# Performance work log

Measured on AMD Instinct MI355X. Metric: run time of the kernel, lower is better.

## Reference

```python
import jax, jax.numpy as jnp
import numpy as np

H, W = 512, 512
# box_info rows: [pad_left, pad_right, pad_top, pad_bottom, box_w, box_h]
BOX_INFO = np.array([
    [0, 256, 0, 256, 256, 256],
    [64, 256, 32, 160, 192, 320],
    [128, 64, 256, 64, 320, 192],
    [300, 84, 300, 84, 128, 128],
    [64, 64, 128, 128, 384, 256],
    [200, 56, 100, 28, 256, 384],
    [32, 320, 256, 32, 160, 224],
    [256, 32, 320, 32, 224, 160]], dtype=np.int64)
BIG = 100000.0


def _conv(x, w, b):
    # 3x3 SAME conv, NCHW / OIHW, followed by ReLU
    y = jax.lax.conv_general_dilated(x, w, window_strides=(1, 1), padding='SAME',
                                     dimension_numbers=('NCHW', 'OIHW', 'NCHW'))
    return jax.nn.relu(y + b[None, :, None, None])


def _block(x, w1, b1, w2, b2, w3, b3):
    return _conv(_conv(_conv(x, w1, b1), w2, b2), w3, b3)


def _resize_and_pad(x, info):
    l, r, t, btm, bw_, bh_ = [int(v) for v in info]
    x = jax.image.resize(x, (x.shape[0], x.shape[1], bh_, bw_), method='bilinear')
    return jnp.pad(x, ((0, 0), (0, 0), (t, btm), (l, r)))


def setup_inputs() -> dict:
    key = jax.random.key(0)
    ks = jax.random.split(key, 8)
    C, U, N = 64, 64, 8
    s = 0.05
    return {
        'instance_feature': jax.random.normal(ks[0], (N, C, 128, 128), jnp.float32),
        'bg_feature': jax.random.normal(ks[1], (1, C, H, W), jnp.float32),
        'iw1': jax.random.normal(ks[2], (U, C, 3, 3), jnp.float32) * s,
        'ib1': jnp.zeros((U,), jnp.float32),
        'iw2': jax.random.normal(ks[3], (U, U, 3, 3), jnp.float32) * s,
        'ib2': jnp.zeros((U,), jnp.float32),
        'iw3': jax.random.normal(ks[4], (1, U, 3, 3), jnp.float32) * s,
        'ib3': jnp.zeros((1,), jnp.float32),
        'bw1': jax.random.normal(ks[5], (U, C, 3, 3), jnp.float32) * s,
        'bb1': jnp.zeros((U,), jnp.float32),
        'bw2': jax.random.normal(ks[6], (U, U, 3, 3), jnp.float32) * s,
        'bb2': jnp.zeros((U,), jnp.float32),
        'bw3': jax.random.normal(ks[7], (1, U, 3, 3), jnp.float32) * s,
        'bb3': jnp.zeros((1,), jnp.float32),
    }


def reference(instance_feature, bg_feature, iw1, ib1, iw2, ib2, iw3, ib3,
              bw1, bb1, bw2, bb2, bw3, bb3):
    n_inst = instance_feature.shape[0]
    masks, fmaps = [], []
    mask_sum = jnp.zeros((1, 1, H, W), bg_feature.dtype)
    for i in range(n_inst):  # static, structurally distinct per-box shapes
        info = BOX_INFO[i]
        l, t, bw_, bh_ = int(info[0]), int(info[2]), int(info[4]), int(info[5])
        crop = instance_feature[i:i + 1]                      # [1,C,h,w]
        pred_mask = _block(crop, iw1, ib1, iw2, ib2, iw3, ib3)  # [1,1,h,w]
        pred_mask = _resize_and_pad(pred_mask, info)           # [1,1,H,W]
        feat = _resize_and_pad(crop, info)                     # [1,C,H,W]
        m = jnp.zeros((1, 1, H, W), bg_feature.dtype).at[:, :, t:t + bh_, l:l + bw_].set(1.0)
        mask_sum = jnp.clip(mask_sum + m, 0.0, 1.0)
        masks.append(pred_mask)
        fmaps.append(feat)
    pred_bg_mask = _block(bg_feature, bw1, bb1, bw2, bb2, bw3, bb3)  # [1,1,H,W]
    masks.append(pred_bg_mask + (1.0 - mask_sum) * BIG)
    mask_cat = jax.nn.softmax(jnp.concatenate(masks, axis=1), axis=1)  # [1,N+1,H,W]
    fm = jnp.concatenate(fmaps + [bg_feature], axis=0)                 # [N+1,C,H,W]
    # weighted blend: sum_n fm[n] * mask[n]
    out = jnp.sum(fm * jnp.transpose(mask_cat, (1, 0, 2, 3)), axis=0, keepdims=True)
    return out
```

## Files before the change

### kernel.cpp

```cpp
#include <hip/hip_runtime.h>
#include <hip/hip_bf16.h>

typedef __hip_bfloat16 bf16;
typedef unsigned short ushort_t;
typedef unsigned int uint32;

typedef short short4_t __attribute__((ext_vector_type(4)));
typedef short short8_t __attribute__((ext_vector_type(8)));
typedef float float4_t __attribute__((ext_vector_type(4)));

union FragU { short4_t h[2]; short8_t v; };
union Frag16 { short8_t v; short s[8]; uint4 u; };

#define BIG 100000.0f

__global__ __launch_bounds__(256) void wtrans(const float* __restrict__ w,
                                              ushort_t* __restrict__ dst)
{
    int idx = blockIdx.x * 256 + threadIdx.x;
    if (idx < 36864) {
        const int i  = idx & 7;
        const int r  = (idx >> 3) & 63;
        const int f  = idx >> 9;
        const int half = f & 1, mb = (f >> 1) & 3, t = f >> 3;
        const int nn = r & 15, qq = r >> 4;
        const int co = mb * 16 + nn;
        const int ci = half * 32 + qq * 8 + i;
        bf16 h = (bf16)w[(co * 64 + ci) * 9 + t];
        dst[idx] = *(ushort_t*)&h;
    }
}

__global__ __launch_bounds__(256) void nchw_to_nhwc(
    const float* __restrict__ in,
    ushort_t* __restrict__ out,
    int H, int W)
{
    __shared__ ushort_t s[64 * 66];
    const int b = blockIdx.z, y = blockIdx.y, x0 = blockIdx.x * 64;
    const int tid = threadIdx.x;
    const long ibase = (long)b * 64 * H * W + (long)y * W + x0;
    {
        const int x = tid & 63, dc = tid >> 6;
        for (int c = dc; c < 64; c += 4) {
            bf16 h = (bf16)in[ibase + (long)c * H * W + x];
            s[c * 66 + x] = *(ushort_t*)&h;
        }
    }
    __syncthreads();
    {
        const int c = tid & 63, dx = tid >> 6;
        const long obase = ((long)b * H * W + (long)y * W + x0) * 64;
        for (int x = dx; x < 64; x += 4)
            out[obase + (long)x * 64 + c] = s[c * 66 + x];
    }
}

__global__ __launch_bounds__(256, 3) void conv3x3_mfma(
    const ushort_t* __restrict__ in,
    ushort_t* __restrict__ out,
    const ushort_t* __restrict__ wt,
    const float* __restrict__ bias,
    int H, int W)
{
    __shared__ ushort_t s_h[2][324 * 36];

    const int b = blockIdx.z;
    const int x0 = blockIdx.x * 16, y0 = blockIdx.y * 16;
    const int tid = threadIdx.x;
    const int lane = tid & 63, wv = tid >> 6;
    const int n = lane & 15, q = lane >> 4;

    const long img = (long)b * H * W;

    for (int idx = tid; idx < 2592; idx += 256) {
        const int p = idx >> 3, c = idx & 7;
        const int py = p / 18, px = p - py * 18;
        const int gy = y0 - 1 + py, gx = x0 - 1 + px;
        uint4 d = {0u, 0u, 0u, 0u};
        if (gy >= 0 && gy < H && gx >= 0 && gx < W)
            d = *(const uint4*)(in + ((img + (long)gy * W + gx) << 6) + c * 8);
        ushort_t* dp = &s_h[c >> 2][p * 36 + (c & 3) * 8];
        *(uint2*)dp       = make_uint2(d.x, d.y);
        *(uint2*)(dp + 4) = make_uint2(d.z, d.w);
    }
    __syncthreads();

    float4_t acc[4][4];
#pragma unroll
    for (int mb = 0; mb < 4; ++mb)
#pragma unroll
        for (int j = 0; j < 4; ++j) acc[mb][j] = (float4_t){0.f, 0.f, 0.f, 0.f};

#pragma unroll
    for (int half = 0; half < 2; ++half) {
        const ushort_t* sh = s_h[half];
#pragma unroll
        for (int t = 0; t < 9; ++t) {
            const int dy = t / 3, dx = t - dy * 3;
            FragU A[4];
#pragma unroll
            for (int mb = 0; mb < 4; ++mb) {
                const ushort_t* ap = wt + (((t * 4 + mb) * 2 + half) << 9) + (lane << 3);
                A[mb].h[0] = *(const short4_t*)ap;
                A[mb].h[1] = *(const short4_t*)(ap + 4);
            }
#pragma unroll
            for (int j = 0; j < 4; ++j) {
                const int row = wv * 4 + j;
                const ushort_t* p = &sh[((row + dy) * 18 + n + dx) * 36 + q * 8];
                FragU B;
                B.h[0] = *(const short4_t*)p;
                B.h[1] = *(const short4_t*)(p + 4);
#pragma unroll
                for (int mb = 0; mb < 4; ++mb)
                    acc[mb][j] = __builtin_amdgcn_mfma_f32_16x16x32_bf16(
                        A[mb].v, B.v, acc[mb][j], 0, 0, 0);
            }
        }
    }

#pragma unroll
    for (int j = 0; j < 4; ++j) {
        const int gy = y0 + wv * 4 + j, gx = x0 + n;
        ushort_t* op0 = out + ((img + (long)gy * W + gx) << 6);
#pragma unroll
        for (int mb = 0; mb < 4; ++mb) {
            const int co = mb * 16 + q * 4;
            const float4 bv = *(const float4*)(bias + co);
            const float bvr[4] = {bv.x, bv.y, bv.z, bv.w};
            bf16 tmp[4];
#pragma unroll
            for (int r = 0; r < 4; ++r) {
                float v = acc[mb][j][r] + bvr[r];
                v = v > 0.f ? v : 0.f;
                tmp[r] = (bf16)v;
            }
            *(uint2*)(op0 + co) = *(uint2*)tmp;
        }
    }
}

__global__ __launch_bounds__(256) void conv3x3_c1(
    const ushort_t* __restrict__ in,
    float* __restrict__ out,
    const float* __restrict__ w,
    const float* __restrict__ bias,
    int H, int W)
{
    __shared__ ushort_t s_in[324 * 72];
    __shared__ float s_w[576];

    const int b = blockIdx.z;
    const int x0 = blockIdx.x * 16, y0 = blockIdx.y * 16;
    const int tid = threadIdx.x;
    for (int k = tid; k < 576; k += 256) s_w[k] = w[k];

    const long img = (long)b * H * W;
    for (int idx = tid; idx < 2592; idx += 256) {
        const int p = idx >> 3, c = idx & 7;
        const int py = p / 18, px = p - py * 18;
        const int gy = y0 - 1 + py, gx = x0 - 1 + px;
        uint4 d = {0u, 0u, 0u, 0u};
        if (gy >= 0 && gy < H && gx >= 0 && gx < W)
            d = *(const uint4*)(in + ((img + (long)gy * W + gx) << 6) + c * 8);
        *(uint4*)&s_in[p * 72 + c * 8] = d;
    }
    __syncthreads();

    const int px = tid & 15, py = tid >> 4;
    float acc = 0.f;
#pragma unroll
    for (int t = 0; t < 9; ++t) {
        const int dy = t / 3, dx = t - dy * 3;
        const ushort_t* p = &s_in[((py + dy) * 18 + px + dx) * 72];
#pragma unroll
        for (int c8 = 0; c8 < 8; ++c8) {
            Frag16 f;
            f.u = *(const uint4*)(p + c8 * 8);
#pragma unroll
            for (int i = 0; i < 8; ++i) {
                float fv = __uint_as_float(((uint32)(ushort_t)f.s[i]) << 16);
                acc += fv * s_w[(c8 * 8 + i) * 9 + t];
            }
        }
    }
    float v = acc + bias[0];
    v = v > 0.f ? v : 0.f;
    out[img + (long)(y0 + py) * W + x0 + px] = v;
}

#define CPB 16

__global__ __launch_bounds__(256) void fuse_out(
    const float* __restrict__ inst,
    const float* __restrict__ bg,
    const float* __restrict__ m,
    const float* __restrict__ bgm,
    float* __restrict__ out)
{
    const int x = blockIdx.x * 256 + threadIdx.x;
    const int y = blockIdx.y;
    const int c0 = blockIdx.z * CPB;

    constexpr int BL[8]  = {0, 64, 128, 300, 64, 200, 32, 256};
    constexpr int BT[8]  = {0, 32, 256, 300, 128, 100, 256, 320};
    constexpr int BBW[8] = {256, 192, 320, 128, 384, 256, 160, 224};
    constexpr int BBH[8] = {256, 320, 192, 128, 256, 384, 224, 160};

    float logits[9];
    int   o00[8], oxs[8], oys[8];
    float wf00[8], wf01[8], wf10[8], wf11[8];
    bool  ins[8];
    bool any = false;

#pragma unroll
    for (int n = 0; n < 8; ++n) {
        const bool inside = (x >= BL[n]) && (x < BL[n] + BBW[n]) &&
                            (y >= BT[n]) && (y < BT[n] + BBH[n]);
        ins[n] = inside;
        float lg = 0.f;
        o00[n] = 0; oxs[n] = 0; oys[n] = 0;
        wf00[n] = wf01[n] = wf10[n] = wf11[n] = 0.f;
        if (inside) {
            any = true;
            float u = ((x - BL[n]) + 0.5f) * (128.0f / BBW[n]) - 0.5f;
            float v = ((y - BT[n]) + 0.5f) * (128.0f / BBH[n]) - 0.5f;
            u = fminf(fmaxf(u, 0.f), 127.f);
            v = fminf(fmaxf(v, 0.f), 127.f);
            int   xx0 = (int)u;  float fx = u - (float)xx0;
            int   yy0 = (int)v;  float fy = v - (float)yy0;
            o00[n] = yy0 * 128 + xx0;
            oxs[n] = (xx0 < 127) ? 1 : 0;
            oys[n] = (yy0 < 127) ? 128 : 0;
            wf00[n] = (1.f - fx) * (1.f - fy);
            wf01[n] = fx * (1.f - fy);
            wf10[n] = (1.f - fx) * fy;
            wf11[n] = fx * fy;
            const float* mp = m + n * 16384;
            lg = wf00[n] * mp[o00[n]] + wf01[n] * mp[o00[n] + oxs[n]] +
                 wf10[n] * mp[o00[n] + oys[n]] +
                 wf11[n] * mp[o00[n] + oxs[n] + oys[n]];
        }
        logits[n] = lg;
    }
    logits[8] = bgm[y * 512 + x] + (any ? 0.f : BIG);

    float mx = logits[0];
#pragma unroll
    for (int i = 1; i < 9; ++i) mx = fmaxf(mx, logits[i]);
    float wgt[9], s = 0.f;
#pragma unroll
    for (int i = 0; i < 9; ++i) { wgt[i] = __expf(logits[i] - mx); s += wgt[i]; }
    const float inv = 1.f / s;
#pragma unroll
    for (int i = 0; i < 9; ++i) wgt[i] *= inv;

#pragma unroll
    for (int n = 0; n < 8; ++n) {
        wf00[n] *= wgt[n]; wf01[n] *= wgt[n];
        wf10[n] *= wgt[n]; wf11[n] *= wgt[n];
    }

    const long pix = (long)y * 512 + x;

    const float* bgp = bg + (long)c0 * 262144 + pix;
    float o[CPB];
#pragma unroll
    for (int cc = 0; cc < CPB; ++cc)
        o[cc] = wgt[8] * bgp[(long)cc * 262144];

#pragma unroll
    for (int n = 0; n < 8; ++n) {
        if (__any((int)ins[n])) {
            const int   ox  = oxs[n], oy = oys[n], oxy = oxs[n] + oys[n];
            const float w00 = wf00[n], w01 = wf01[n];
            const float w10 = wf10[n], w11 = wf11[n];
            const float* p = inst + (long)(n * 64 + c0) * 16384 + o00[n];
#pragma unroll
            for (int cc = 0; cc < CPB; ++cc) {
                o[cc] += w00 * p[0]  + w01 * p[ox] +
                         w10 * p[oy] + w11 * p[oxy];
                p += 16384;
            }
        }
    }

    float* outp = out + (long)c0 * 262144 + pix;
#pragma unroll
    for (int cc = 0; cc < CPB; ++cc)
        __builtin_nontemporal_store(o[cc], outp + (long)cc * 262144);
}

extern "C" void kernel_launch(void* const* d_in, const int* in_sizes, int n_in,
                              void* d_out, int out_size, void* d_ws, size_t ws_size,
                              hipStream_t stream)
{
    (void)in_sizes; (void)n_in; (void)out_size; (void)ws_size;

    const float* instf = (const float*)d_in[0];
    const float* bgf   = (const float*)d_in[1];
    const float* iw1   = (const float*)d_in[2];
    const float* ib1   = (const float*)d_in[3];
    const float* iw2   = (const float*)d_in[4];
    const float* ib2   = (const float*)d_in[5];
    const float* iw3   = (const float*)d_in[6];
    const float* ib3   = (const float*)d_in[7];
    const float* bw1   = (const float*)d_in[8];
    const float* bb1   = (const float*)d_in[9];
    const float* bw2   = (const float*)d_in[10];
    const float* bb2   = (const float*)d_in[11];
    const float* bw3   = (const float*)d_in[12];
    const float* bb3   = (const float*)d_in[13];

    char* ws = (char*)d_ws;
    ushort_t* instN = (ushort_t*)(ws);
    ushort_t* y2    = (ushort_t*)(ws + 16777216);
    ushort_t* y1    = (ushort_t*)(ws + 33554432);
    ushort_t* bgN   = (ushort_t*)(ws);
    ushort_t* bg1   = (ushort_t*)(ws + 33554432);
    ushort_t* bg2   = (ushort_t*)(ws);
    float*    minst  = (float*)(ws + 67108864);
    float*    bgmask = (float*)(ws + 67633152);
    ushort_t* wt0 = (ushort_t*)(ws + 67633152);
    ushort_t* wt1 = wt0 + 36864;
    ushort_t* wt2 = wt0 + 2 * 36864;
    ushort_t* wt3 = wt0 + 3 * 36864;

    wtrans<<<144, 256, 0, stream>>>(iw1, wt0);
    wtrans<<<144, 256, 0, stream>>>(iw2, wt1);
    wtrans<<<144, 256, 0, stream>>>(bw1, wt2);
    wtrans<<<144, 256, 0, stream>>>(bw2, wt3);

    nchw_to_nhwc<<<dim3(2, 128, 8), 256, 0, stream>>>(instf, instN, 128, 128);
    conv3x3_mfma<<<dim3(8, 8, 8), 256, 0, stream>>>(instN, y1, wt0, ib1, 128, 128);
    conv3x3_mfma<<<dim3(8, 8, 8), 256, 0, stream>>>(y1, y2, wt1, ib2, 128, 128);
    conv3x3_c1  <<<dim3(8, 8, 8), 256, 0, stream>>>(y2, minst, iw3, ib3, 128, 128);

    nchw_to_nhwc<<<dim3(8, 512, 1), 256, 0, stream>>>(bgf, bgN, 512, 512);
    conv3x3_mfma<<<dim3(32, 32, 1), 256, 0, stream>>>(bgN, bg1, wt2, bb1, 512, 512);
    conv3x3_mfma<<<dim3(32, 32, 1), 256, 0, stream>>>(bg1, bg2, wt3, bb2, 512, 512);
    conv3x3_c1  <<<dim3(32, 32, 1), 256, 0, stream>>>(bg2, bgmask, bw3, bb3, 512, 512);

    fuse_out<<<dim3(2, 512, 4), 256, 0, stream>>>(instf, bgf, minst, bgmask, (float*)d_out);
}
```

Before: 405.4 us.

## Merge prep kernels and fuse instance final conv with bg layout transform

Folds the four weight-transform launches and the instance NCHW-to-NHWC transpose into one prep kernel. Merges the instance single-output conv with the background NCHW-to-NHWC transpose into one launch that branches on block id, and remaps the workspace buffers so these stages do not overwrite each other. This cuts launch count and lets independent small stages share the GPU instead of running serially. It also lowers the conv launch-bounds occupancy hint from 3 to 2, trading occupancy for more registers per thread.

```diff
diff --git a/kernel.cpp b/kernel.cpp
--- a/kernel.cpp
+++ b/kernel.cpp
@@ -14,11 +14,22 @@
 
 #define BIG 100000.0f
 
-__global__ __launch_bounds__(256) void wtrans(const float* __restrict__ w,
-                                              ushort_t* __restrict__ dst)
-{
-    int idx = blockIdx.x * 256 + threadIdx.x;
-    if (idx < 36864) {
+__global__ __launch_bounds__(256) void prep(
+    const float* __restrict__ instf,
+    ushort_t* __restrict__ instN,
+    const float* __restrict__ w0, const float* __restrict__ w1,
+    const float* __restrict__ w2, const float* __restrict__ w3,
+    ushort_t* __restrict__ wt)
+{
+    __shared__ ushort_t s[64 * 66];
+    const int id = blockIdx.x;
+    const int tid = threadIdx.x;
+
+    if (id >= 2048) {
+        const int gidx = (id - 2048) * 256 + tid;
+        const int set = gidx / 36864;
+        const int idx = gidx - set * 36864;
+        const float* w = (set == 0) ? w0 : (set == 1) ? w1 : (set == 2) ? w2 : w3;
         const int i  = idx & 7;
         const int r  = (idx >> 3) & 63;
         const int f  = idx >> 9;
@@ -27,36 +38,30 @@
         const int co = mb * 16 + nn;
         const int ci = half * 32 + qq * 8 + i;
         bf16 h = (bf16)w[(co * 64 + ci) * 9 + t];
-        dst[idx] = *(ushort_t*)&h;
-    }
-}
-
-__global__ __launch_bounds__(256) void nchw_to_nhwc(
-    const float* __restrict__ in,
-    ushort_t* __restrict__ out,
-    int H, int W)
-{
-    __shared__ ushort_t s[64 * 66];
-    const int b = blockIdx.z, y = blockIdx.y, x0 = blockIdx.x * 64;
-    const int tid = threadIdx.x;
-    const long ibase = (long)b * 64 * H * W + (long)y * W + x0;
+        wt[set * 36864 + idx] = *(ushort_t*)&h;
+        return;
+    }
+
+    const int b = id >> 8, r = id & 255;
+    const int y = r >> 1, x0 = (r & 1) * 64;
+    const long ibase = (long)b * 64 * 16384 + (long)y * 128 + x0;
     {
         const int x = tid & 63, dc = tid >> 6;
         for (int c = dc; c < 64; c += 4) {
-            bf16 h = (bf16)in[ibase + (long)c * H * W + x];
+            bf16 h = (bf16)instf[ibase + (long)c * 16384 + x];
             s[c * 66 + x] = *(ushort_t*)&h;
         }
     }
     __syncthreads();
     {
         const int c = tid & 63, dx = tid >> 6;
-        const long obase = ((long)b * H * W + (long)y * W + x0) * 64;
+        const long obase = ((long)b * 16384 + (long)y * 128 + x0) * 64;
         for (int x = dx; x < 64; x += 4)
-            out[obase + (long)x * 64 + c] = s[c * 66 + x];
-    }
-}
-
-__global__ __launch_bounds__(256, 3) void conv3x3_mfma(
+            instN[obase + (long)x * 64 + c] = s[c * 66 + x];
+    }
+}
+
+__global__ __launch_bounds__(256, 2) void conv3x3_mfma(
     const ushort_t* __restrict__ in,
     ushort_t* __restrict__ out,
     const ushort_t* __restrict__ wt,
@@ -139,6 +144,80 @@
             *(uint2*)(op0 + co) = *(uint2*)tmp;
         }
     }
+}
+
+__global__ __launch_bounds__(256) void c1i_nchwb(
+    const ushort_t* __restrict__ y2in,
+    float* __restrict__ minst,
+    const float* __restrict__ w,
+    const float* __restrict__ bias,
+    const float* __restrict__ bgf,
+    ushort_t* __restrict__ bgN)
+{
+    __shared__ __align__(16) char smem[48960];
+    const int id = blockIdx.x, tid = threadIdx.x;
+
+    if (id >= 512) {
+        ushort_t* s = (ushort_t*)smem;
+        const int r = id - 512;
+        const int y = r >> 3, x0 = (r & 7) * 64;
+        const long ibase = (long)y * 512 + x0;
+        {
+            const int x = tid & 63, dc = tid >> 6;
+            for (int c = dc; c < 64; c += 4) {
+                bf16 h = (bf16)bgf[ibase + (long)c * 262144 + x];
+                s[c * 66 + x] = *(ushort_t*)&h;
+            }
+        }
+        __syncthreads();
+        {
+            const int c = tid & 63, dx = tid >> 6;
+            const long obase = ((long)y * 512 + x0) * 64;
+            for (int x = dx; x < 64; x += 4)
+                bgN[obase + (long)x * 64 + c] = s[c * 66 + x];
+        }
+        return;
+    }
+
+    ushort_t* s_in = (ushort_t*)smem;
+    float*    s_w  = (float*)(smem + 46656);
+
+    const int b = id >> 6, r = id & 63;
+    const int y0 = (r >> 3) * 16, x0 = (r & 7) * 16;
+    for (int k = tid; k < 576; k += 256) s_w[k] = w[k];
+
+    const long img = (long)b * 16384;
+    for (int idx = tid; idx < 2592; idx += 256) {
+        const int p = idx >> 3, c = idx & 7;
+        const int py = p / 18, px = p - py * 18;
+        const int gy = y0 - 1 + py, gx = x0 - 1 + px;
+        uint4 d = {0u, 0u, 0u, 0u};
+        if (gy >= 0 && gy < 128 && gx >= 0 && gx < 128)
+            d = *(const uint4*)(y2in + ((img + (long)gy * 128 + gx) << 6) + c * 8);
+        *(uint4*)&s_in[p * 72 + c * 8] = d;
+    }
+    __syncthreads();
+
+    const int px = tid & 15, py = tid >> 4;
+    float acc = 0.f;
+#pragma unroll
+    for (int t = 0; t < 9; ++t) {
+        const int dy = t / 3, dx = t - dy * 3;
+        const ushort_t* p = &s_in[((py + dy) * 18 + px + dx) * 72];
+#pragma unroll
+        for (int c8 = 0; c8 < 8; ++c8) {
+            Frag16 f;
+            f.u = *(const uint4*)(p + c8 * 8);
+#pragma unroll
+            for (int i = 0; i < 8; ++i) {
+                float fv = __uint_as_float(((uint32)(ushort_t)f.s[i]) << 16);
+                acc += fv * s_w[(c8 * 8 + i) * 9 + t];
+            }
+        }
+    }
+    float v = acc + bias[0];
+    v = v > 0.f ? v : 0.f;
+    minst[img + (long)(y0 + py) * 128 + x0 + px] = v;
 }
 
 __global__ __launch_bounds__(256) void conv3x3_c1(
@@ -315,11 +394,11 @@
 
     char* ws = (char*)d_ws;
     ushort_t* instN = (ushort_t*)(ws);
-    ushort_t* y2    = (ushort_t*)(ws + 16777216);
-    ushort_t* y1    = (ushort_t*)(ws + 33554432);
-    ushort_t* bgN   = (ushort_t*)(ws);
-    ushort_t* bg1   = (ushort_t*)(ws + 33554432);
-    ushort_t* bg2   = (ushort_t*)(ws);
+    ushort_t* y1    = (ushort_t*)(ws + 16777216);
+    ushort_t* y2    = (ushort_t*)(ws);
+    ushort_t* bgN   = (ushort_t*)(ws + 33554432);
+    ushort_t* bg1   = (ushort_t*)(ws);
+    ushort_t* bg2   = (ushort_t*)(ws + 33554432);
     float*    minst  = (float*)(ws + 67108864);
     float*    bgmask = (float*)(ws + 67633152);
     ushort_t* wt0 = (ushort_t*)(ws + 67633152);
@@ -327,20 +406,12 @@
     ushort_t* wt2 = wt0 + 2 * 36864;
     ushort_t* wt3 = wt0 + 3 * 36864;
 
-    wtrans<<<144, 256, 0, stream>>>(iw1, wt0);
-    wtrans<<<144, 256, 0, stream>>>(iw2, wt1);
-    wtrans<<<144, 256, 0, stream>>>(bw1, wt2);
-    wtrans<<<144, 256, 0, stream>>>(bw2, wt3);
-
-    nchw_to_nhwc<<<dim3(2, 128, 8), 256, 0, stream>>>(instf, instN, 128, 128);
+    prep<<<2624, 256, 0, stream>>>(instf, instN, iw1, iw2, bw1, bw2, wt0);
     conv3x3_mfma<<<dim3(8, 8, 8), 256, 0, stream>>>(instN, y1, wt0, ib1, 128, 128);
     conv3x3_mfma<<<dim3(8, 8, 8), 256, 0, stream>>>(y1, y2, wt1, ib2, 128, 128);
-    conv3x3_c1  <<<dim3(8, 8, 8), 256, 0, stream>>>(y2, minst, iw3, ib3, 128, 128);
-
-    nchw_to_nhwc<<<dim3(8, 512, 1), 256, 0, stream>>>(bgf, bgN, 512, 512);
+    c1i_nchwb<<<4608, 256, 0, stream>>>(y2, minst, iw3, ib3, bgf, bgN);
     conv3x3_mfma<<<dim3(32, 32, 1), 256, 0, stream>>>(bgN, bg1, wt2, bb1, 512, 512);
     conv3x3_mfma<<<dim3(32, 32, 1), 256, 0, stream>>>(bg1, bg2, wt3, bb2, 512, 512);
     conv3x3_c1  <<<dim3(32, 32, 1), 256, 0, stream>>>(bg2, bgmask, bw3, bb3, 512, 512);
-
     fuse_out<<<dim3(2, 512, 4), 256, 0, stream>>>(instf, bgf, minst, bgmask, (float*)d_out);
 }
```

After: 394.4 us. 2.7% less time.
